# Kernel optimization log

Measured on AMD Instinct MI355X. Metric: run time of the kernel, lower is better.

The kernel has to match this reference:

```python
import jax, jax.numpy as jnp
from jax import lax
import numpy as np

H = 256        # hidden_dim
PRED_LEN = 96  # pred_len
B, L = 256, 512


def _gru_step(h, xt, W_ih, W_hh, b_ih, b_hh):
    # PyTorch GRU gate math. xt: [B, in], h: [B, H], W_ih: [3H, in], W_hh: [3H, H]
    gi = xt @ W_ih.T + b_ih            # [B, 3H]
    gh = h @ W_hh.T + b_hh             # [B, 3H]
    i_r, i_z, i_n = jnp.split(gi, 3, axis=-1)
    h_r, h_z, h_n = jnp.split(gh, 3, axis=-1)
    r = jax.nn.sigmoid(i_r + h_r)
    z = jax.nn.sigmoid(i_z + h_z)
    n = jnp.tanh(i_n + r * h_n)
    return (1.0 - z) * n + z * h


def _run_gru_layer(xs, W_ih, W_hh, b_ih, b_hh):
    # xs: [L, B, in] -> (ys [L, B, H], h_last [B, H])
    h0 = jnp.zeros((xs.shape[1], H), xs.dtype)
    def step(h, xt):
        hn = _gru_step(h, xt, W_ih, W_hh, b_ih, b_hh)
        return hn, hn
    h_last, ys = lax.scan(step, h0, xs)
    return ys, h_last


def setup_inputs() -> dict:
    key = jax.random.key(0)
    ks = jax.random.split(key, 16)
    s = 1.0 / np.sqrt(H)
    u = lambda k, shape: jax.random.uniform(k, shape, jnp.float32, -s, s)
    return {
        "x": jax.random.normal(ks[0], (B, 1, L), jnp.float32),
        # encoder GRU layer 0 (input_size=1)
        "W_ih0": u(ks[1], (3 * H, 1)), "W_hh0": u(ks[2], (3 * H, H)),
        "b_ih0": u(ks[3], (3 * H,)), "b_hh0": u(ks[4], (3 * H,)),
        # encoder GRU layer 1 (input_size=H)
        "W_ih1": u(ks[5], (3 * H, H)), "W_hh1": u(ks[6], (3 * H, H)),
        "b_ih1": u(ks[7], (3 * H,)), "b_hh1": u(ks[8], (3 * H,)),
        # decoder GRUCell (input_size=1)
        "Wd_ih": u(ks[9], (3 * H, 1)), "Wd_hh": u(ks[10], (3 * H, H)),
        "bd_ih": u(ks[11], (3 * H,)), "bd_hh": u(ks[12], (3 * H,)),
        # output Linear(H, 1)
        "Wo": u(ks[13], (1, H)), "bo": u(ks[14], (1,)),
    }


def reference(x, W_ih0, W_hh0, b_ih0, b_hh0, W_ih1, W_hh1, b_ih1, b_hh1,
              Wd_ih, Wd_hh, bd_ih, bd_hh, Wo, bo):
    # seq = x[:, 0, :].unsqueeze(-1) -> [B, L, 1]; scan wants [L, B, 1]
    xs = jnp.transpose(x[:, 0, :, None], (1, 0, 2))
    ys0, _ = _run_gru_layer(xs, W_ih0, W_hh0, b_ih0, b_hh0)
    _, h_t = _run_gru_layer(ys0, W_ih1, W_hh1, b_ih1, b_hh1)  # h_n[-1]: [B, H]
    # (dropout between layers is inactive in eval mode)

    dec_in0 = jnp.zeros((x.shape[0], 1), x.dtype)

    def dec_step(carry, _):
        h, inp = carry
        h = _gru_step(h, inp, Wd_ih, Wd_hh, bd_ih, bd_hh)
        step = h @ Wo.T + bo           # [B, 1]
        return (h, step), step

    _, steps = lax.scan(dec_step, (h_t, dec_in0), None, length=PRED_LEN)
    # steps: [pred_len, B, 1] -> cat along dim 1 -> [B, pred_len]
    return jnp.transpose(steps[..., 0], (1, 0))
```

## Files before the change

kernel.cpp:

```cpp
#include <hip/hip_runtime.h>
#include <hip/hip_fp16.h>

#define HDIM 256
#define LSEQ 512
#define PRED 96
#define NTHR 512

typedef _Float16 f16x8 __attribute__((ext_vector_type(8)));
typedef _Float16 f16x4 __attribute__((ext_vector_type(4)));
typedef float f32x4 __attribute__((ext_vector_type(4)));
typedef unsigned int u32;

__device__ __forceinline__ float sigm(float x) { return 1.f / (1.f + __expf(-x)); }
__device__ __forceinline__ float tanh_(float x) { float t = __expf(2.f * x); return 1.f - 2.f / (t + 1.f); }
__device__ __forceinline__ float dppx1(float v) {
  return __builtin_bit_cast(float, __builtin_amdgcn_update_dpp(
      0, __builtin_bit_cast(int, v), 0xB1, 0xF, 0xF, true));
}

struct __align__(16) DynS {
  _Float16 A[16][4096];
  _Float16 h[2][2][256];
  float tw[3][256], tb[3][256], bnh[256], wo[256];
  float xv[LSEQ];
  float redd[2][8];
};

#define CAST_A(DST, SRC) asm("" : "=a"(DST) : "0"(SRC))

__device__ __forceinline__ f16x8 cvt8(const float* p) {
  const float4 a0 = *(const float4*)p;
  const float4 a1 = *(const float4*)(p + 4);
  f16x8 tf;
  tf[0] = (_Float16)a0.x; tf[1] = (_Float16)a0.y;
  tf[2] = (_Float16)a0.z; tf[3] = (_Float16)a0.w;
  tf[4] = (_Float16)a1.x; tf[5] = (_Float16)a1.y;
  tf[6] = (_Float16)a1.z; tf[7] = (_Float16)a1.w;
  return tf;
}

#define DECL8                                                                  \
  f32x4 ac[6];                 \
  f32x4 zc;                                                                    \
  { f32x4 z4 = {0.f, 0.f, 0.f, 0.f}; asm("" : "=a"(zc) : "0"(z4)); }           \
  f16x8 Aa[4][8];

#define LOADA_REG(WPTR)                                                        \
  _Pragma("unroll") for (int tau = 0; tau < 4; ++tau)                          \
  _Pragma("unroll") for (int kt = 0; kt < 8; ++kt) {                           \
    const f16x8 tf = cvt8((WPTR) +                                             \
        (size_t)(256 * (tau >> 1) + 32 * w + 16 * (tau & 1) + n) * HDIM +      \
        32 * kt + 8 * q);                                                      \
    CAST_A(Aa[tau][kt], tf);                                                   \
  }

#define STAGEA(WPTR)                                                           \
  _Pragma("unroll") for (int j = 0; j < 2; ++j)                                \
  _Pragma("unroll") for (int kt = 0; kt < 8; ++kt) {                           \
    const f16x8 tf = cvt8((WPTR) +                                             \
        (size_t)(512 + 32 * w + 16 * j + n) * HDIM + 32 * kt + 8 * q);         \
    *(f16x8*)(sm.A[w * 2 + j] + kt * 512 + n * 32 + q * 8) = tf;               \
  }

#define MM_A_S(I, AF, B) asm volatile("v_mfma_f32_16x16x32_f16 %0, %1, %2, %3" : "=a"(ac[I]) : "a"(AF), "v"(B), "a"(zc));
#define MM_A(I, AF, B)   asm volatile("v_mfma_f32_16x16x32_f16 %0, %1, %2, %0" : "+a"(ac[I]) : "a"(AF), "v"(B));
#define MM_V_S(I, AF, B) asm volatile("v_mfma_f32_16x16x32_f16 %0, %1, %2, %3" : "=a"(ac[I]) : "v"(AF), "v"(B), "a"(zc));
#define MM_V(I, AF, B)   asm volatile("v_mfma_f32_16x16x32_f16 %0, %1, %2, %0" : "+a"(ac[I]) : "v"(AF), "v"(B));

#define KQ_S(KT)                                                               \
  { const f16x8 u = *(const f16x8*)(hp + (KT) * 64);                           \
    const f16x8 l0 = *(const f16x8*)(aw0 + (KT) * 512);                        \
    const f16x8 l1 = *(const f16x8*)(aw1 + (KT) * 512);                        \
    MM_A_S(0, Aa[0][KT], u) MM_A_S(1, Aa[1][KT], u)                            \
    MM_A_S(2, Aa[2][KT], u) MM_A_S(3, Aa[3][KT], u)                            \
    MM_V_S(4, l0, u) MM_V_S(5, l1, u) }
#define KQ(KT)                                                                 \
  { const f16x8 u = *(const f16x8*)(hp + (KT) * 64);                           \
    const f16x8 l0 = *(const f16x8*)(aw0 + (KT) * 512);                        \
    const f16x8 l1 = *(const f16x8*)(aw1 + (KT) * 512);                        \
    MM_A(0, Aa[0][KT], u) MM_A(1, Aa[1][KT], u)                                \
    MM_A(2, Aa[2][KT], u) MM_A(3, Aa[3][KT], u)                                \
    MM_V(4, l0, u) MM_V(5, l1, u) }

#define FENCE                                                                  \
  asm volatile("s_nop 7\n\ts_nop 7\n\ts_nop 7\n\ts_nop 7\n\t"                  \
               "s_nop 7\n\ts_nop 7\n\ts_nop 7\n\ts_nop 7"                      \
               : "+a"(ac[0]), "+a"(ac[1]), "+a"(ac[2]),                        \
                 "+a"(ac[3]), "+a"(ac[4]), "+a"(ac[5]));                       \
  __builtin_amdgcn_sched_barrier(0);

#define BAR asm volatile("s_waitcnt lgkmcnt(0)\n\ts_barrier" ::: "memory")

#define SELG2(P, G)                                                            \
  { const f32x4 e0 = ac[2 * (G)], e1 = ac[2 * (G) + 1]; P = s1 ? e1 : e0; }
#define PSUM(P)                                                                \
  { P[0] += dppx1(P[0]); P[1] += dppx1(P[1]);                                  \
    P[2] += dppx1(P[2]); P[3] += dppx1(P[3]); }

#define MCORE8(PB, ...)                                                        \
  {                                                                            \
    const char* hp = hq + (PB) * 1024;                                         \
    __VA_ARGS__                                                                \
    KQ_S(0) KQ(1) KQ(2) KQ(3) KQ(4) KQ(5) KQ(6) KQ(7)                          \
    FENCE                                                                      \
    SELG2(pr, 0) PSUM(pr)                                                      \
    SELG2(pz, 1) PSUM(pz)                                                      \
    SELG2(pn, 2) PSUM(pn)                                                      \
  }

#define GTAIL8(GR, GZ, GN, RHOOK, STEXTRA)                                     \
  {                                                                            \
    const char* rh = hrow + pb * 1024;                                         \
    char* wh = hrow + (pb ^ 1) * 1024;                                         \
    const f16x4 hh = *(const f16x4*)rh;                                        \
    const f16x4 hl = *(const f16x4*)(rh + 512);                                \
    const f32x4 bn4 = *(const f32x4*)bnrow;                                    \
    f16x4 vh, vl;                                                              \
    _Pragma("unroll") for (int r = 0; r < 4; ++r) {                            \
      const float rr = sigm((GR)[r] + pr[r]);                                  \
      const float zz = sigm((GZ)[r] + pz[r]);                                  \
      const float nn = tanh_(fmaf(rr, pn[r] + bn4[r], (GN)[r]));               \
      const float ho = (float)hh[r] + (float)hl[r];                            \
      const float hv = fmaf(zz, ho - nn, nn);                                  \
      vh[r] = (_Float16)hv;                                                    \
      vl[r] = (_Float16)(hv - (float)vh[r]);                                   \
      RHOOK                                                                    \
    }                                                                          \
    if (st) {                                                                  \
      *(f16x4*)wh = vh;                                                        \
      *(f16x4*)(wh + 512) = vl;                                                \
      STEXTRA                                                                  \
    }                                                                          \
  }

#define LANE_GEOM8                                                             \
  const int tid = threadIdx.x;                                                 \
  const int w = tid >> 6, lane = tid & 63, n = lane & 15, q = lane >> 4;       \
  const int b = blockIdx.x;                                                    \
  const bool s1 = (n & 2) != 0;                                                \
  const bool st = (n & 13) == 0;      \
  const int sg1 = (n >> 1) & 1;                                                \
  const int row = 32 * w + 16 * sg1 + 4 * q;                                   \
  const char* hq = (const char*)sm.h + (n & 1) * 512 + q * 16;                 \
  char* hrow = (char*)sm.h + row * 2;                                          \
  const char* bnrow = (const char*)sm.bnh + row * 4;                           \
  const _Float16* aw0 = sm.A[w * 2] + n * 32 + q * 8;                          \
  const _Float16* aw1 = sm.A[w * 2 + 1] + n * 32 + q * 8;

__global__ __attribute__((amdgpu_flat_work_group_size(NTHR, NTHR), amdgpu_waves_per_eu(2, 2)))
void gru_l0(const float* __restrict__ x, const float* __restrict__ Wih0,
            const float* __restrict__ Whh0, const float* __restrict__ bih0,
            const float* __restrict__ bhh0, __half* __restrict__ ys) {
  extern __shared__ char smem_[];
  DynS& sm = *reinterpret_cast<DynS*>(smem_);
  LANE_GEOM8
  DECL8
  const char* twp = (const char*)sm.tw + row * 4;
  const char* tbp = (const char*)sm.tb + row * 4;

  sm.xv[tid] = x[(size_t)b * LSEQ + tid];
  if (tid < 256) {
#pragma unroll
    for (int g = 0; g < 3; ++g) {
      sm.tw[g][tid] = Wih0[256 * g + tid];
      sm.tb[g][tid] = bih0[256 * g + tid] + (g < 2 ? bhh0[256 * g + tid] : 0.f);
    }
    sm.bnh[tid] = bhh0[512 + tid];
  }
  ((u32*)sm.h)[tid] = 0;
  STAGEA(Whh0);
  LOADA_REG(Whh0);
  __syncthreads();

  __half* ysp = ys + (size_t)b * LSEQ * HDIM + row;
  int pb = 0;
#pragma unroll 1
  for (int t = 0; t < LSEQ; ++t) {
    const float xt = sm.xv[t];
    f32x4 pr, pz, pn;
    MCORE8(pb, ;)
    const f32x4 g_r = *(const f32x4*)twp * xt + *(const f32x4*)tbp;
    const f32x4 g_z = *(const f32x4*)(twp + 1024) * xt + *(const f32x4*)(tbp + 1024);
    const f32x4 g_n = *(const f32x4*)(twp + 2048) * xt + *(const f32x4*)(tbp + 2048);
    GTAIL8(g_r, g_z, g_n, ;, *(f16x4*)ysp = vh;)
    ysp += HDIM;
    pb ^= 1;
    BAR;
  }
}

__global__ __launch_bounds__(256) void gemm_gi(
    const float* __restrict__ Wih1, const float* __restrict__ bih1,
    const float* __restrict__ bhh1, const __half* __restrict__ ys,
    __half* __restrict__ gi) {
  const int lane = threadIdx.x & 63;
  const int wv = threadIdx.x >> 6;
  const size_t bt0 = (size_t)blockIdx.x << 4;
  const int n = lane & 15, q = lane >> 4;

  f16x8 bfr[8];
  const __half* yrow = ys + (bt0 + n) * HDIM + q * 8;
#pragma unroll
  for (int kk = 0; kk < 8; ++kk) bfr[kk] = *(const f16x8*)(yrow + kk * 32);

#pragma unroll 1
  for (int mt = 0; mt < 12; ++mt) {
    const int j0 = (wv * 12 + mt) << 4;
    const float* arow = Wih1 + (size_t)(j0 + n) * HDIM + q * 8;
    f32x4 acc = {0.f, 0.f, 0.f, 0.f};
#pragma unroll
    for (int kk = 0; kk < 8; ++kk) {
      const f16x8 af = cvt8(arow + kk * 32);
      acc = __builtin_amdgcn_mfma_f32_16x16x32_f16(af, bfr[kk], acc, 0, 0, 0);
    }
    const int jr = j0 + (q << 2);
    __half o4[4];
#pragma unroll
    for (int r2 = 0; r2 < 4; ++r2) {
      const float bb = bih1[jr + r2] + (j0 < 512 ? bhh1[jr + r2] : 0.f);
      o4[r2] = __float2half(acc[r2] + bb);
    }
    *(uint2*)(gi + (bt0 + n) * 768 + jr) = *(uint2*)o4;
  }
}

#define LOADGI(PF, T)                                                          \
  { const __half* gp = gi + ((size_t)b * LSEQ + (T)) * 768 + row;              \
    PF[0] = *(const uint2*)(gp);                                               \
    PF[1] = *(const uint2*)(gp + 256);                                         \
    PF[2] = *(const uint2*)(gp + 512); }

__global__ __attribute__((amdgpu_flat_work_group_size(NTHR, NTHR), amdgpu_waves_per_eu(2, 2)))
void gru_l1dec(const float* __restrict__ Whh1, const float* __restrict__ bhh1,
               const float* __restrict__ Wdih, const float* __restrict__ Wdhh,
               const float* __restrict__ bdih, const float* __restrict__ bdhh,
               const float* __restrict__ Wo, const float* __restrict__ bo,
               const __half* __restrict__ gi, float* __restrict__ outp) {
  extern __shared__ char smem_[];
  DynS& sm = *reinterpret_cast<DynS*>(smem_);
  LANE_GEOM8
  DECL8
  const char* twp = (const char*)sm.tw + row * 4;
  const char* tbp = (const char*)sm.tb + row * 4;
  const char* wop = (const char*)sm.wo + row * 4;

  if (tid < 256) sm.bnh[tid] = bhh1[512 + tid];
  ((u32*)sm.h)[tid] = 0;
  STAGEA(Whh1);
  LOADA_REG(Whh1);
  __syncthreads();

  int pb = 0;
#pragma unroll 1
  for (int t = 0; t < LSEQ; ++t) {
    uint2 pf[3];
    f32x4 pr, pz, pn;
    MCORE8(pb, LOADGI(pf, t))
    const __half2* p0 = (const __half2*)&pf[0];
    const __half2* p1 = (const __half2*)&pf[1];
    const __half2* p2 = (const __half2*)&pf[2];
    const float2 r01 = __half22float2(p0[0]), r23 = __half22float2(p0[1]);
    const float2 z01 = __half22float2(p1[0]), z23 = __half22float2(p1[1]);
    const float2 n01 = __half22float2(p2[0]), n23 = __half22float2(p2[1]);
    const f32x4 g_r = {r01.x, r01.y, r23.x, r23.y};
    const f32x4 g_z = {z01.x, z01.y, z23.x, z23.y};
    const f32x4 g_n = {n01.x, n01.y, n23.x, n23.y};
    GTAIL8(g_r, g_z, g_n, ;, ;)
    pb ^= 1;
    BAR;
  }

  const float bov = bo[0];
  STAGEA(Wdhh);
  LOADA_REG(Wdhh);
  if (tid < 256) {
#pragma unroll
    for (int g = 0; g < 3; ++g) {
      sm.tw[g][tid] = Wdih[256 * g + tid];
      sm.tb[g][tid] = bdih[256 * g + tid] + (g < 2 ? bdhh[256 * g + tid] : 0.f);
    }
    sm.bnh[tid] = bdhh[512 + tid];
    sm.wo[tid] = Wo[tid];
  }
  if (tid < 8) sm.redd[0][tid] = (tid == 0) ? -bov : 0.f;
  __syncthreads();

  int rb = 0;
#pragma unroll 1
  for (int t = 0; t < PRED; ++t) {
    const f32x4 rd0 = *(const f32x4*)sm.redd[rb];
    const f32x4 rd1 = *(const f32x4*)(&sm.redd[rb][4]);
    const float it = bov + rd0[0] + rd0[1] + rd0[2] + rd0[3] +
                     rd1[0] + rd1[1] + rd1[2] + rd1[3];
    if (tid == 0 && t > 0) outp[(size_t)b * PRED + t - 1] = it;
    f32x4 pr, pz, pn;
    MCORE8(pb, ;)
    const f32x4 g_r = *(const f32x4*)twp * it + *(const f32x4*)tbp;
    const f32x4 g_z = *(const f32x4*)(twp + 1024) * it + *(const f32x4*)(tbp + 1024);
    const f32x4 g_n = *(const f32x4*)(twp + 2048) * it + *(const f32x4*)(tbp + 2048);
    const f32x4 wo4 = *(const f32x4*)wop;
    float c = 0.f;
    GTAIL8(g_r, g_z, g_n, c = fmaf(wo4[r], hv, c);, ;)
    if (!st) c = 0.f;
    c += __shfl_xor(c, 2);
    c += __shfl_xor(c, 16);
    c += __shfl_xor(c, 32);
    if (lane == 0) sm.redd[rb ^ 1][w] = c;
    pb ^= 1;
    rb ^= 1;
    BAR;
  }
  if (tid == 0) {
    float ov = bov;
#pragma unroll
    for (int ww = 0; ww < 8; ++ww) ov += sm.redd[rb][ww];
    outp[(size_t)b * PRED + PRED - 1] = ov;
  }
}

extern "C" void kernel_launch(void* const* d_in, const int* in_sizes, int n_in,
                              void* d_out, int out_size, void* d_ws, size_t ws_size,
                              hipStream_t stream) {
  const float* x    = (const float*)d_in[0];
  const float* Wih0 = (const float*)d_in[1];
  const float* Whh0 = (const float*)d_in[2];
  const float* bih0 = (const float*)d_in[3];
  const float* bhh0 = (const float*)d_in[4];
  const float* Wih1 = (const float*)d_in[5];
  const float* Whh1 = (const float*)d_in[6];
  const float* bih1 = (const float*)d_in[7];
  const float* bhh1 = (const float*)d_in[8];
  const float* Wdih = (const float*)d_in[9];
  const float* Wdhh = (const float*)d_in[10];
  const float* bdih = (const float*)d_in[11];
  const float* bdhh = (const float*)d_in[12];
  const float* Wo   = (const float*)d_in[13];
  const float* bo   = (const float*)d_in[14];

  __half* ys = (__half*)d_ws;
  __half* gi = ys + (size_t)256 * 512 * 256;

  static int attr_done = 0;
  if (!attr_done) {
    (void)hipFuncSetAttribute((const void*)gru_l0,
        hipFuncAttributeMaxDynamicSharedMemorySize, (int)sizeof(DynS));
    (void)hipFuncSetAttribute((const void*)gru_l1dec,
        hipFuncAttributeMaxDynamicSharedMemorySize, (int)sizeof(DynS));
    attr_done = 1;
  }

  gru_l0<<<256, NTHR, sizeof(DynS), stream>>>(x, Wih0, Whh0, bih0, bhh0, ys);
  gemm_gi<<<(256 * 512) / 16, 256, 0, stream>>>(Wih1, bih1, bhh1, ys, gi);
  gru_l1dec<<<256, NTHR, sizeof(DynS), stream>>>(Whh1, bhh1, Wdih, Wdhh,
                                                 bdih, bdhh, Wo, bo, gi,
                                                 (float*)d_out);
}
```

Before: 3.157 ms.

## Split gate epilogue across twice as many lanes and swizzle LDS weight layout

The gate nonlinearity epilogue now has each storing lane handle 2 rows instead of 4, so twice as many lanes share the serial per-step sigmoid/tanh work. The lane-select, stores, gi loads and output reduction are adjusted to match, including an extra shuffle. Separately, the LDS-staged weight fragments are XOR-swizzled by lane to reduce bank conflicts on the per-step LDS reads. This shortens the latency-bound critical path of each recurrent step, at the cost of more lanes doing redundant selection work and one more cross-lane reduction step.

```diff
diff --git a/kernel.cpp b/kernel.cpp
--- a/kernel.cpp
+++ b/kernel.cpp
@@ -7,8 +7,9 @@
 #define NTHR 512
 
 typedef _Float16 f16x8 __attribute__((ext_vector_type(8)));
-typedef _Float16 f16x4 __attribute__((ext_vector_type(4)));
+typedef _Float16 f16x2 __attribute__((ext_vector_type(2)));
 typedef float f32x4 __attribute__((ext_vector_type(4)));
+typedef float f32x2 __attribute__((ext_vector_type(2)));
 typedef unsigned int u32;
 
 __device__ __forceinline__ float sigm(float x) { return 1.f / (1.f + __expf(-x)); }
@@ -16,6 +17,11 @@
 __device__ __forceinline__ float dppx1(float v) {
   return __builtin_bit_cast(float, __builtin_amdgcn_update_dpp(
       0, __builtin_bit_cast(int, v), 0xB1, 0xF, 0xF, true));
+}
+__device__ __forceinline__ f32x2 cvt2f(u32 v) {
+  const __half2 h = __builtin_bit_cast(__half2, v);
+  const float2 f = __half22float2(h);
+  f32x2 r; r[0] = f.x; r[1] = f.y; return r;
 }
 
 struct __align__(16) DynS {
@@ -59,7 +65,7 @@
   _Pragma("unroll") for (int kt = 0; kt < 8; ++kt) {                           \
     const f16x8 tf = cvt8((WPTR) +                                             \
         (size_t)(512 + 32 * w + 16 * j + n) * HDIM + 32 * kt + 8 * q);         \
-    *(f16x8*)(sm.A[w * 2 + j] + kt * 512 + n * 32 + q * 8) = tf;               \
+    *(f16x8*)(sm.A[w * 2 + j] + kt * 512 + n * 32 + qs * 8) = tf;              \
   }
 
 #define MM_A_S(I, AF, B) asm volatile("v_mfma_f32_16x16x32_f16 %0, %1, %2, %3" : "=a"(ac[I]) : "a"(AF), "v"(B), "a"(zc));
@@ -91,11 +97,12 @@
 
 #define BAR asm volatile("s_waitcnt lgkmcnt(0)\n\ts_barrier" ::: "memory")
 
-#define SELG2(P, G)                                                            \
-  { const f32x4 e0 = ac[2 * (G)], e1 = ac[2 * (G) + 1]; P = s1 ? e1 : e0; }
-#define PSUM(P)                                                                \
-  { P[0] += dppx1(P[0]); P[1] += dppx1(P[1]);                                  \
-    P[2] += dppx1(P[2]); P[3] += dppx1(P[3]); }
+#define SELP(P, G)                                                             \
+  { const f32x4 e0 = ac[2 * (G)], e1 = ac[2 * (G) + 1];                        \
+    const f32x4 t = s1 ? e1 : e0;                                              \
+    P[0] = s2 ? t[2] : t[0];                                                   \
+    P[1] = s2 ? t[3] : t[1]; }
+#define PSUM2(P) { P[0] += dppx1(P[0]); P[1] += dppx1(P[1]); }
 
 #define MCORE8(PB, ...)                                                        \
   {                                                                            \
@@ -103,23 +110,23 @@
     __VA_ARGS__                                                                \
     KQ_S(0) KQ(1) KQ(2) KQ(3) KQ(4) KQ(5) KQ(6) KQ(7)                          \
     FENCE                                                                      \
-    SELG2(pr, 0) PSUM(pr)                                                      \
-    SELG2(pz, 1) PSUM(pz)                                                      \
-    SELG2(pn, 2) PSUM(pn)                                                      \
+    SELP(pr, 0) PSUM2(pr)                                                      \
+    SELP(pz, 1) PSUM2(pz)                                                      \
+    SELP(pn, 2) PSUM2(pn)                                                      \
   }
 
 #define GTAIL8(GR, GZ, GN, RHOOK, STEXTRA)                                     \
   {                                                                            \
     const char* rh = hrow + pb * 1024;                                         \
     char* wh = hrow + (pb ^ 1) * 1024;                                         \
-    const f16x4 hh = *(const f16x4*)rh;                                        \
-    const f16x4 hl = *(const f16x4*)(rh + 512);                                \
-    const f32x4 bn4 = *(const f32x4*)bnrow;                                    \
-    f16x4 vh, vl;                                                              \
-    _Pragma("unroll") for (int r = 0; r < 4; ++r) {                            \
+    const f16x2 hh = *(const f16x2*)rh;                                        \
+    const f16x2 hl = *(const f16x2*)(rh + 512);                                \
+    const f32x2 bn2 = *(const f32x2*)bnrow;                                    \
+    f16x2 vh, vl;                                                              \
+    _Pragma("unroll") for (int r = 0; r < 2; ++r) {                            \
       const float rr = sigm((GR)[r] + pr[r]);                                  \
       const float zz = sigm((GZ)[r] + pz[r]);                                  \
-      const float nn = tanh_(fmaf(rr, pn[r] + bn4[r], (GN)[r]));               \
+      const float nn = tanh_(fmaf(rr, pn[r] + bn2[r], (GN)[r]));               \
       const float ho = (float)hh[r] + (float)hl[r];                            \
       const float hv = fmaf(zz, ho - nn, nn);                                  \
       vh[r] = (_Float16)hv;                                                    \
@@ -127,8 +134,8 @@
       RHOOK                                                                    \
     }                                                                          \
     if (st) {                                                                  \
-      *(f16x4*)wh = vh;                                                        \
-      *(f16x4*)(wh + 512) = vl;                                                \
+      *(f16x2*)wh = vh;                                                        \
+      *(f16x2*)(wh + 512) = vl;                                                \
       STEXTRA                                                                  \
     }                                                                          \
   }
@@ -137,15 +144,18 @@
   const int tid = threadIdx.x;                                                 \
   const int w = tid >> 6, lane = tid & 63, n = lane & 15, q = lane >> 4;       \
   const int b = blockIdx.x;                                                    \
-  const bool s1 = (n & 2) != 0;                                                \
-  const bool st = (n & 13) == 0;      \
+  const bool s1 = (n & 2) != 0;                          \
+  const bool s2 = (n & 4) != 0;                 \
+  const bool st = (n & 9) == 0;      \
   const int sg1 = (n >> 1) & 1;                                                \
+  const int rp = (n >> 2) & 1;                                                 \
   const int row = 32 * w + 16 * sg1 + 4 * q;                                   \
+  const int qs = q ^ ((n >> 1) & 3);             \
   const char* hq = (const char*)sm.h + (n & 1) * 512 + q * 16;                 \
-  char* hrow = (char*)sm.h + row * 2;                                          \
-  const char* bnrow = (const char*)sm.bnh + row * 4;                           \
-  const _Float16* aw0 = sm.A[w * 2] + n * 32 + q * 8;                          \
-  const _Float16* aw1 = sm.A[w * 2 + 1] + n * 32 + q * 8;
+  char* hrow = (char*)sm.h + row * 2 + rp * 4;                                 \
+  const char* bnrow = (const char*)sm.bnh + row * 4 + rp * 8;                  \
+  const _Float16* aw0 = sm.A[w * 2] + n * 32 + qs * 8;                         \
+  const _Float16* aw1 = sm.A[w * 2 + 1] + n * 32 + qs * 8;
 
 __global__ __attribute__((amdgpu_flat_work_group_size(NTHR, NTHR), amdgpu_waves_per_eu(2, 2)))
 void gru_l0(const float* __restrict__ x, const float* __restrict__ Wih0,
@@ -155,8 +165,8 @@
   DynS& sm = *reinterpret_cast<DynS*>(smem_);
   LANE_GEOM8
   DECL8
-  const char* twp = (const char*)sm.tw + row * 4;
-  const char* tbp = (const char*)sm.tb + row * 4;
+  const char* twp = (const char*)sm.tw + row * 4 + rp * 8;
+  const char* tbp = (const char*)sm.tb + row * 4 + rp * 8;
 
   sm.xv[tid] = x[(size_t)b * LSEQ + tid];
   if (tid < 256) {
@@ -172,17 +182,17 @@
   LOADA_REG(Whh0);
   __syncthreads();
 
-  __half* ysp = ys + (size_t)b * LSEQ * HDIM + row;
+  _Float16* ysp = (_Float16*)ys + (size_t)b * LSEQ * HDIM + row + rp * 2;
   int pb = 0;
 #pragma unroll 1
   for (int t = 0; t < LSEQ; ++t) {
     const float xt = sm.xv[t];
-    f32x4 pr, pz, pn;
+    f32x2 pr, pz, pn;
     MCORE8(pb, ;)
-    const f32x4 g_r = *(const f32x4*)twp * xt + *(const f32x4*)tbp;
-    const f32x4 g_z = *(const f32x4*)(twp + 1024) * xt + *(const f32x4*)(tbp + 1024);
-    const f32x4 g_n = *(const f32x4*)(twp + 2048) * xt + *(const f32x4*)(tbp + 2048);
-    GTAIL8(g_r, g_z, g_n, ;, *(f16x4*)ysp = vh;)
+    const f32x2 g_r = *(const f32x2*)twp * xt + *(const f32x2*)tbp;
+    const f32x2 g_z = *(const f32x2*)(twp + 1024) * xt + *(const f32x2*)(tbp + 1024);
+    const f32x2 g_n = *(const f32x2*)(twp + 2048) * xt + *(const f32x2*)(tbp + 2048);
+    GTAIL8(g_r, g_z, g_n, ;, *(f16x2*)ysp = vh;)
     ysp += HDIM;
     pb ^= 1;
     BAR;
@@ -225,10 +235,10 @@
 }
 
 #define LOADGI(PF, T)                                                          \
-  { const __half* gp = gi + ((size_t)b * LSEQ + (T)) * 768 + row;              \
-    PF[0] = *(const uint2*)(gp);                                               \
-    PF[1] = *(const uint2*)(gp + 256);                                         \
-    PF[2] = *(const uint2*)(gp + 512); }
+  { const __half* gp = gi + ((size_t)b * LSEQ + (T)) * 768 + row + rp * 2;     \
+    PF[0] = *(const u32*)(gp);                                                 \
+    PF[1] = *(const u32*)(gp + 256);                                           \
+    PF[2] = *(const u32*)(gp + 512); }
 
 __global__ __attribute__((amdgpu_flat_work_group_size(NTHR, NTHR), amdgpu_waves_per_eu(2, 2)))
 void gru_l1dec(const float* __restrict__ Whh1, const float* __restrict__ bhh1,
@@ -240,9 +250,9 @@
   DynS& sm = *reinterpret_cast<DynS*>(smem_);
   LANE_GEOM8
   DECL8
-  const char* twp = (const char*)sm.tw + row * 4;
-  const char* tbp = (const char*)sm.tb + row * 4;
-  const char* wop = (const char*)sm.wo + row * 4;
+  const char* twp = (const char*)sm.tw + row * 4 + rp * 8;
+  const char* tbp = (const char*)sm.tb + row * 4 + rp * 8;
+  const char* wop = (const char*)sm.wo + row * 4 + rp * 8;
 
   if (tid < 256) sm.bnh[tid] = bhh1[512 + tid];
   ((u32*)sm.h)[tid] = 0;
@@ -253,18 +263,12 @@
   int pb = 0;
 #pragma unroll 1
   for (int t = 0; t < LSEQ; ++t) {
-    uint2 pf[3];
-    f32x4 pr, pz, pn;
+    u32 pf[3];
+    f32x2 pr, pz, pn;
     MCORE8(pb, LOADGI(pf, t))
-    const __half2* p0 = (const __half2*)&pf[0];
-    const __half2* p1 = (const __half2*)&pf[1];
-    const __half2* p2 = (const __half2*)&pf[2];
-    const float2 r01 = __half22float2(p0[0]), r23 = __half22float2(p0[1]);
-    const float2 z01 = __half22float2(p1[0]), z23 = __half22float2(p1[1]);
-    const float2 n01 = __half22float2(p2[0]), n23 = __half22float2(p2[1]);
-    const f32x4 g_r = {r01.x, r01.y, r23.x, r23.y};
-    const f32x4 g_z = {z01.x, z01.y, z23.x, z23.y};
-    const f32x4 g_n = {n01.x, n01.y, n23.x, n23.y};
+    const f32x2 g_r = cvt2f(pf[0]);
+    const f32x2 g_z = cvt2f(pf[1]);
+    const f32x2 g_n = cvt2f(pf[2]);
     GTAIL8(g_r, g_z, g_n, ;, ;)
     pb ^= 1;
     BAR;
@@ -293,16 +297,17 @@
     const float it = bov + rd0[0] + rd0[1] + rd0[2] + rd0[3] +
                      rd1[0] + rd1[1] + rd1[2] + rd1[3];
     if (tid == 0 && t > 0) outp[(size_t)b * PRED + t - 1] = it;
-    f32x4 pr, pz, pn;
+    f32x2 pr, pz, pn;
     MCORE8(pb, ;)
-    const f32x4 g_r = *(const f32x4*)twp * it + *(const f32x4*)tbp;
-    const f32x4 g_z = *(const f32x4*)(twp + 1024) * it + *(const f32x4*)(tbp + 1024);
-    const f32x4 g_n = *(const f32x4*)(twp + 2048) * it + *(const f32x4*)(tbp + 2048);
-    const f32x4 wo4 = *(const f32x4*)wop;
+    const f32x2 g_r = *(const f32x2*)twp * it + *(const f32x2*)tbp;
+    const f32x2 g_z = *(const f32x2*)(twp + 1024) * it + *(const f32x2*)(tbp + 1024);
+    const f32x2 g_n = *(const f32x2*)(twp + 2048) * it + *(const f32x2*)(tbp + 2048);
+    const f32x2 wo2 = *(const f32x2*)wop;
     float c = 0.f;
-    GTAIL8(g_r, g_z, g_n, c = fmaf(wo4[r], hv, c);, ;)
+    GTAIL8(g_r, g_z, g_n, c = fmaf(wo2[r], hv, c);, ;)
     if (!st) c = 0.f;
     c += __shfl_xor(c, 2);
+    c += __shfl_xor(c, 4);
     c += __shfl_xor(c, 16);
     c += __shfl_xor(c, 32);
     if (lane == 0) sm.redd[rb ^ 1][w] = c;
```

After: 2.646 ms. -16.2%, faster.
